# Optimization experiments

Measured on AMD Instinct MI355X. Metric: run time of the kernel, lower is better.

Reference implementation:

```python
import jax, jax.numpy as jnp
import numpy as np

B, C, H, W = 64, 3, 512, 512


def setup_inputs() -> dict:
    key = jax.random.key(0)
    k1, k2, k3 = jax.random.split(key, 3)
    img = jax.random.normal(k1, (B, C, H, W), dtype=jnp.float32)
    rot = jax.random.normal(k2, (B,), dtype=jnp.float32)          # radians
    trans = jax.random.normal(k3, (B, 2), dtype=jnp.float32) * 0.1
    scale = jnp.ones((B,), dtype=jnp.float32)
    return {"img": img, "rot": rot, "trans": trans, "scale": scale}


def reference(img, rot, trans, scale):
    # Batched equivalent of the per-image loop:
    #   theta = [[cos/s, -sin/s, tx], [sin/s, cos/s, ty]]  (2x3 per image)
    #   grid  = F.affine_grid(theta, img.size())           (align_corners=False)
    #   out   = F.grid_sample(img, grid)                    (bilinear, zeros pad)
    b_, c_, h_, w_ = img.shape
    cs = jnp.cos(rot) / scale
    sn = jnp.sin(rot) / scale

    # Base normalized grid (align_corners=False): x_i = (2i+1)/W - 1
    xs = (2.0 * jnp.arange(w_, dtype=img.dtype) + 1.0) / w_ - 1.0
    ys = (2.0 * jnp.arange(h_, dtype=img.dtype) + 1.0) / h_ - 1.0
    gy, gx = jnp.meshgrid(ys, xs, indexing="ij")  # [H, W]

    # Apply affine: [gx', gy'] = theta @ [gx, gy, 1]
    gx_t = cs[:, None, None] * gx + (-sn)[:, None, None] * gy + trans[:, 0, None, None]
    gy_t = sn[:, None, None] * gx + cs[:, None, None] * gy + trans[:, 1, None, None]

    # Unnormalize (align_corners=False): ix = ((g+1)*W - 1)/2
    ix = ((gx_t + 1.0) * w_ - 1.0) * 0.5
    iy = ((gy_t + 1.0) * h_ - 1.0) * 0.5

    x0 = jnp.floor(ix)
    y0 = jnp.floor(iy)
    wx1 = ix - x0  # frac weights
    wy1 = iy - y0
    x0i = x0.astype(jnp.int32)
    y0i = y0.astype(jnp.int32)

    bidx = jnp.arange(b_)[:, None, None]  # [B,1,1]

    def corner(yi, xi, w):
        valid = (xi >= 0) & (xi < w_) & (yi >= 0) & (yi < h_)
        yc = jnp.clip(yi, 0, h_ - 1)
        xc = jnp.clip(xi, 0, w_ - 1)
        v = img[bidx, :, yc, xc]  # [B,H,W,C] gather
        return v * (w * valid)[..., None]

    out = (
        corner(y0i, x0i, (1.0 - wy1) * (1.0 - wx1))
        + corner(y0i, x0i + 1, (1.0 - wy1) * wx1)
        + corner(y0i + 1, x0i, wy1 * (1.0 - wx1))
        + corner(y0i + 1, x0i + 1, wy1 * wx1)
    )
    return jnp.transpose(out, (0, 3, 1, 2))  # [B,C,H,W]
```

## Files before the change

kernel.cpp:

```cpp
#include <hip/hip_runtime.h>
#include <stdint.h>

#define BB 64
#define CC 3
#define HH 512
#define WW 512
#define TILE 32
#define MAXBH 48
#define MAXBW 52
#define LSTR 53

typedef float f32x2 __attribute__((ext_vector_type(2)));

__device__ __forceinline__ void pix2in(float x, float y,
                                       float cs, float sn, float tx, float ty,
                                       float& ix, float& iy)
{
    float gx = (2.0f * x + 1.0f) * (1.0f / (float)WW) - 1.0f;
    float gy = (2.0f * y + 1.0f) * (1.0f / (float)HH) - 1.0f;
    float gxt = cs * gx - sn * gy + tx;
    float gyt = sn * gx + cs * gy + ty;
    ix = ((gxt + 1.0f) * (float)WW - 1.0f) * 0.5f;
    iy = ((gyt + 1.0f) * (float)HH - 1.0f) * 0.5f;
}

__global__ __launch_bounds__(256) void warp_setup(
    const float* __restrict__ rot, const float* __restrict__ trans,
    const float* __restrict__ scale, float* __restrict__ ws)
{
    const int i = blockIdx.x * 256 + threadIdx.x;
    const int b = i >> 8, t = i & 255;
    const float r = rot[b];
    const float inv_s = 1.0f / scale[b];
    const float cs = cosf(r) * inv_s;
    const float sn = sinf(r) * inv_s;
    const float tx = trans[2 * b], ty = trans[2 * b + 1];
    if (t == 0)
        reinterpret_cast<float4*>(ws)[b] = make_float4(cs, sn, tx, ty);

    const int oy0 = (t >> 4) * TILE;
    const int ox0 = (t & 15) * TILE;
    float ixa, iya, ixb, iyb, ixc, iyc, ixd, iyd;
    pix2in((float)ox0,              (float)oy0,              cs, sn, tx, ty, ixa, iya);
    pix2in((float)(ox0 + TILE - 1), (float)oy0,              cs, sn, tx, ty, ixb, iyb);
    pix2in((float)ox0,              (float)(oy0 + TILE - 1), cs, sn, tx, ty, ixc, iyc);
    pix2in((float)(ox0 + TILE - 1), (float)(oy0 + TILE - 1), cs, sn, tx, ty, ixd, iyd);
    const float minix = fminf(fminf(ixa, ixb), fminf(ixc, ixd));
    const float maxix = fmaxf(fmaxf(ixa, ixb), fmaxf(ixc, ixd));
    const float miniy = fminf(fminf(iya, iyb), fminf(iyc, iyd));
    const float maxiy = fmaxf(fmaxf(iya, iyb), fmaxf(iyc, iyd));
    const int bx0 = (int)floorf(minix) - 1;
    const int bx1 = (int)floorf(maxix) + 2;
    const int by0 = (int)floorf(miniy) - 1;
    const int by1 = (int)floorf(maxiy) + 2;
    int bx0c = bx0 & ~3;
    const int bw = bx1 - bx0c + 1;
    const int bh = by1 - by0 + 1;

    const uint32_t fit      = (bw <= MAXBW && bh <= MAXBH) ? 1u : 0u;
    const uint32_t interior = (bx0c >= 0 && bx1 < WW && by0 >= 0 && by1 < HH) ? 1u : 0u;
    const int bx0s = min(max(bx0c, -2048), 2047);
    const int by0s = min(max(by0,  -2048), 2047);
    const int bhs  = min(bh, 63);
    const uint32_t desc = ((uint32_t)bx0s & 0xFFFu)
                        | (((uint32_t)by0s & 0xFFFu) << 12)
                        | ((uint32_t)bhs << 24)
                        | (fit << 30) | (interior << 31);
    reinterpret_cast<uint32_t*>(ws)[256 + i] = desc;
}

template <bool INTERIOR>
__device__ __forceinline__ void compute_store(
    const float (*lds)[MAXBH][LSTR], float* __restrict__ outb,
    int tid, int ox0, int oy0, int bx0c, int by0,
    float cs, float sn, float tpx, float tpy, long plane)
{
    const int row = tid >> 4;
    const int xp  = (tid & 15) * 2;
    const int oy  = oy0 + row;
    const int oxb = ox0 + xp;

    float ix0, iy0;
    pix2in((float)oxb, (float)oy, cs, sn, tpx, tpy, ix0, iy0);

    f32x2 res[CC];
    #pragma unroll
    for (int e = 0; e < 2; ++e) {
        const float ix = fmaf((float)e, cs, ix0);
        const float iy = fmaf((float)e, sn, iy0);
        const float x0f = floorf(ix), y0f = floorf(iy);
        const float wx1 = ix - x0f,  wy1 = iy - y0f;
        const float wx0 = 1.0f - wx1, wy0 = 1.0f - wy1;
        const int x0 = (int)x0f, y0 = (int)y0f;

        float w00 = wy0 * wx0, w01 = wy0 * wx1, w10 = wy1 * wx0, w11 = wy1 * wx1;
        if (!INTERIOR) {
            const int x1 = x0 + 1, y1 = y0 + 1;
            const float vx0 = (x0 >= 0 && x0 < WW) ? 1.0f : 0.0f;
            const float vx1 = (x1 >= 0 && x1 < WW) ? 1.0f : 0.0f;
            const float vy0 = (y0 >= 0 && y0 < HH) ? 1.0f : 0.0f;
            const float vy1 = (y1 >= 0 && y1 < HH) ? 1.0f : 0.0f;
            w00 *= vy0 * vx0; w01 *= vy0 * vx1; w10 *= vy1 * vx0; w11 *= vy1 * vx1;
        }

        const int idx = (y0 - by0) * LSTR + (x0 - bx0c);
        #pragma unroll
        for (int c = 0; c < CC; ++c) {
            const float* pb = &lds[c][0][0] + idx;
            res[c][e] = w00 * pb[0] + w01 * pb[1]
                      + w10 * pb[LSTR] + w11 * pb[LSTR + 1];
        }
    }
    const long ob = (long)oy * WW + oxb;
    #pragma unroll
    for (int c = 0; c < CC; ++c)
        __builtin_nontemporal_store(res[c],
            reinterpret_cast<f32x2*>(outb + (long)c * plane + ob));
}

__global__ __launch_bounds__(512) void warp_tiled(
    const float* __restrict__ img, const float* __restrict__ ws,
    float* __restrict__ out)
{
    __shared__ float lds[CC][MAXBH][LSTR];

    const int g   = blockIdx.x;
    const int swz = (g & 7) * ((BB * 256) / 8) + (g >> 3);
    const int b   = swz >> 8;
    const int t   = swz & 255;
    const int oy0 = (t >> 4) * TILE;
    const int ox0 = (t & 15) * TILE;

    const float4 p = reinterpret_cast<const float4*>(ws)[b];
    const float cs = p.x, sn = p.y, tpx = p.z, tpy = p.w;
    const uint32_t desc = reinterpret_cast<const uint32_t*>(ws)[256 + swz];
    const int  bx0c     = ((int)(desc << 20)) >> 20;
    const int  by0      = ((int)(desc << 8))  >> 20;
    const int  bh       = (desc >> 24) & 63;
    const bool fit      = (desc >> 30) & 1;
    const bool interior = (desc >> 31) & 1;

    const long plane = (long)HH * WW;
    const float* imb = img + (long)b * CC * plane;
    float* outb      = out + (long)b * CC * plane;
    const int tid = threadIdx.x;

    if (fit) {
        const int q  = tid >> 4;
        const int ql = tid & 15;
        if (ql < 13) {
            if (interior) {
                const float* prow = imb + (long)(by0 + q) * WW + bx0c + ql * 4;
                #pragma unroll
                for (int c = 0; c < CC; ++c) {
                    const float* pr = prow + (long)c * plane;
                    if (q < bh) {
                        const float4 v = *reinterpret_cast<const float4*>(pr);
                        float* dst = &lds[c][q][ql * 4];
                        dst[0] = v.x; dst[1] = v.y; dst[2] = v.z; dst[3] = v.w;
                    }
                    if (q + 32 < bh) {
                        const float4 v = *reinterpret_cast<const float4*>(pr + 32 * WW);
                        float* dst = &lds[c][q + 32][ql * 4];
                        dst[0] = v.x; dst[1] = v.y; dst[2] = v.z; dst[3] = v.w;
                    }
                }
            } else {
                #pragma unroll
                for (int c = 0; c < CC; ++c) {
                    const float* pc = imb + (long)c * plane;
                    for (int r = q; r < bh; r += 32) {
                        const int grow = by0 + r;
                        const int gcol = bx0c + ql * 4;
                        float4 v = make_float4(0.f, 0.f, 0.f, 0.f);
                        if (grow >= 0 && grow < HH) {
                            const float* prow = pc + (long)grow * WW;
                            if (gcol >= 0 && gcol <= WW - 4) {
                                v = *reinterpret_cast<const float4*>(prow + gcol);
                            } else {
                                int gc0 = gcol, gc1 = gcol + 1, gc2 = gcol + 2, gc3 = gcol + 3;
                                v.x = (gc0 >= 0 && gc0 < WW) ? prow[gc0] : 0.f;
                                v.y = (gc1 >= 0 && gc1 < WW) ? prow[gc1] : 0.f;
                                v.z = (gc2 >= 0 && gc2 < WW) ? prow[gc2] : 0.f;
                                v.w = (gc3 >= 0 && gc3 < WW) ? prow[gc3] : 0.f;
                            }
                        }
                        float* dst = &lds[c][r][ql * 4];
                        dst[0] = v.x; dst[1] = v.y; dst[2] = v.z; dst[3] = v.w;
                    }
                }
            }
        }
        __syncthreads();

        if (interior)
            compute_store<true >(lds, outb, tid, ox0, oy0, bx0c, by0, cs, sn, tpx, tpy, plane);
        else
            compute_store<false>(lds, outb, tid, ox0, oy0, bx0c, by0, cs, sn, tpx, tpy, plane);
    } else {
        #pragma unroll
        for (int k = 0; k < 2; ++k) {
            const int pidx = tid + k * 512;
            const int py = pidx >> 5;
            const int px = pidx & 31;
            const int ox = ox0 + px, oy = oy0 + py;

            float ix, iy;
            pix2in((float)ox, (float)oy, cs, sn, tpx, tpy, ix, iy);
            const float x0f = floorf(ix), y0f = floorf(iy);
            const float wx1 = ix - x0f,  wy1 = iy - y0f;
            const int x0 = (int)x0f, y0 = (int)y0f;
            const int x1 = x0 + 1,  y1 = y0 + 1;

            const float vx0 = (x0 >= 0 && x0 < WW) ? 1.0f : 0.0f;
            const float vx1 = (x1 >= 0 && x1 < WW) ? 1.0f : 0.0f;
            const float vy0 = (y0 >= 0 && y0 < HH) ? 1.0f : 0.0f;
            const float vy1 = (y1 >= 0 && y1 < HH) ? 1.0f : 0.0f;

            const int x0c = min(max(x0, 0), WW - 1);
            const int x1c = min(max(x1, 0), WW - 1);
            const int y0c = min(max(y0, 0), HH - 1);
            const int y1c = min(max(y1, 0), HH - 1);

            const float w00 = (1.0f - wy1) * (1.0f - wx1) * vy0 * vx0;
            const float w01 = (1.0f - wy1) * wx1          * vy0 * vx1;
            const float w10 = wy1          * (1.0f - wx1) * vy1 * vx0;
            const float w11 = wy1          * wx1          * vy1 * vx1;

            const int o00 = y0c * WW + x0c, o01 = y0c * WW + x1c;
            const int o10 = y1c * WW + x0c, o11 = y1c * WW + x1c;
            const int ob = oy * WW + ox;
            #pragma unroll
            for (int c = 0; c < CC; ++c) {
                const float* pc = imb + (long)c * plane;
                const float v = w00 * pc[o00] + w01 * pc[o01]
                              + w10 * pc[o10] + w11 * pc[o11];
                __builtin_nontemporal_store(v, &outb[(long)c * plane + ob]);
            }
        }
    }
}

extern "C" void kernel_launch(void* const* d_in, const int* in_sizes, int n_in,
                              void* d_out, int out_size, void* d_ws, size_t ws_size,
                              hipStream_t stream) {
    const float* img   = (const float*)d_in[0];
    const float* rot   = (const float*)d_in[1];
    const float* trans = (const float*)d_in[2];
    const float* scale = (const float*)d_in[3];
    float* out = (float*)d_out;
    float* ws  = (float*)d_ws;

    warp_setup<<<dim3(BB), 256, 0, stream>>>(rot, trans, scale, ws);
    warp_tiled<<<dim3(BB * 256), 512, 0, stream>>>(img, ws, out);
}
```

Measured before the change: 77.68 us.

## Interleave channels in LDS as float4 texels with XOR swizzle

Changes the shared-memory tile from three planar channel arrays into one interleaved array of float4 texels (RGB plus padding), stored with an XOR swizzle to spread bank accesses. Each bilinear tap now takes a single 128-bit LDS read for all three channels instead of three scalar reads, so the number of LDS instructions in the sampling loop drops. The cost is a larger LDS footprint (a padding lane per texel), which may reduce occupancy, plus a transpose during the tile load. The edge-case load path now also does scalar global loads per element.

New measurement: 76.90 us. Within noise of the previous version (-1.0%).

```diff
diff --git a/kernel.cpp b/kernel.cpp
--- a/kernel.cpp
+++ b/kernel.cpp
@@ -8,9 +8,10 @@
 #define TILE 32
 #define MAXBH 48
 #define MAXBW 52
-#define LSTR 53
+#define RS 58
 
 typedef float f32x2 __attribute__((ext_vector_type(2)));
+typedef float f32x4 __attribute__((ext_vector_type(4)));
 
 __device__ __forceinline__ void pix2in(float x, float y,
                                        float cs, float sn, float tx, float ty,
@@ -71,7 +72,7 @@
 
 template <bool INTERIOR>
 __device__ __forceinline__ void compute_store(
-    const float (*lds)[MAXBH][LSTR], float* __restrict__ outb,
+    const f32x4 (*lds)[RS], float* __restrict__ outb,
     int tid, int ox0, int oy0, int bx0c, int by0,
     float cs, float sn, float tpx, float tpy, long plane)
 {
@@ -83,7 +84,7 @@
     float ix0, iy0;
     pix2in((float)oxb, (float)oy, cs, sn, tpx, tpy, ix0, iy0);
 
-    f32x2 res[CC];
+    f32x4 acc0, acc1;
     #pragma unroll
     for (int e = 0; e < 2; ++e) {
         const float ix = fmaf((float)e, cs, ix0);
@@ -103,26 +104,34 @@
             w00 *= vy0 * vx0; w01 *= vy0 * vx1; w10 *= vy1 * vx0; w11 *= vy1 * vx1;
         }
 
-        const int idx = (y0 - by0) * LSTR + (x0 - bx0c);
-        #pragma unroll
-        for (int c = 0; c < CC; ++c) {
-            const float* pb = &lds[c][0][0] + idx;
-            res[c][e] = w00 * pb[0] + w01 * pb[1]
-                      + w10 * pb[LSTR] + w11 * pb[LSTR + 1];
-        }
+        const int lx0 = x0 - bx0c;
+        const int lx1 = lx0 + 1;
+        const int ly0 = y0 - by0;
+        const int s0  = lx0 ^ ((lx0 >> 2) & 7);
+        const int s1  = lx1 ^ ((lx1 >> 2) & 7);
+
+        const f32x4 p00 = lds[ly0][s0];
+        const f32x4 p01 = lds[ly0][s1];
+        const f32x4 p10 = lds[ly0 + 1][s0];
+        const f32x4 p11 = lds[ly0 + 1][s1];
+
+        const f32x4 r4 = w00 * p00 + w01 * p01 + w10 * p10 + w11 * p11;
+        if (e == 0) acc0 = r4; else acc1 = r4;
     }
     const long ob = (long)oy * WW + oxb;
-    #pragma unroll
-    for (int c = 0; c < CC; ++c)
-        __builtin_nontemporal_store(res[c],
-            reinterpret_cast<f32x2*>(outb + (long)c * plane + ob));
+    const f32x2 o0 = {acc0.x, acc1.x};
+    const f32x2 o1 = {acc0.y, acc1.y};
+    const f32x2 o2 = {acc0.z, acc1.z};
+    __builtin_nontemporal_store(o0, reinterpret_cast<f32x2*>(outb + ob));
+    __builtin_nontemporal_store(o1, reinterpret_cast<f32x2*>(outb + plane + ob));
+    __builtin_nontemporal_store(o2, reinterpret_cast<f32x2*>(outb + 2 * plane + ob));
 }
 
 __global__ __launch_bounds__(512) void warp_tiled(
     const float* __restrict__ img, const float* __restrict__ ws,
     float* __restrict__ out)
 {
-    __shared__ float lds[CC][MAXBH][LSTR];
+    __shared__ f32x4 lds[MAXBH][RS];
 
     const int g   = blockIdx.x;
     const int swz = (g & 7) * ((BB * 256) / 8) + (g >> 3);
@@ -149,44 +158,35 @@
         const int q  = tid >> 4;
         const int ql = tid & 15;
         if (ql < 13) {
-            if (interior) {
-                const float* prow = imb + (long)(by0 + q) * WW + bx0c + ql * 4;
-                #pragma unroll
-                for (int c = 0; c < CC; ++c) {
-                    const float* pr = prow + (long)c * plane;
-                    if (q < bh) {
-                        const float4 v = *reinterpret_cast<const float4*>(pr);
-                        float* dst = &lds[c][q][ql * 4];
-                        dst[0] = v.x; dst[1] = v.y; dst[2] = v.z; dst[3] = v.w;
-                    }
-                    if (q + 32 < bh) {
-                        const float4 v = *reinterpret_cast<const float4*>(pr + 32 * WW);
-                        float* dst = &lds[c][q + 32][ql * 4];
-                        dst[0] = v.x; dst[1] = v.y; dst[2] = v.z; dst[3] = v.w;
-                    }
+            const int sb = (ql * 4) ^ (ql & 7);
+            if (interior && (bx0c + 51 < WW)) {
+                for (int r = q; r < bh; r += 32) {
+                    const float* pr = imb + (long)(by0 + r) * WW + (bx0c + ql * 4);
+                    const float4 a  = *reinterpret_cast<const float4*>(pr);
+                    const float4 bv = *reinterpret_cast<const float4*>(pr + plane);
+                    const float4 cv = *reinterpret_cast<const float4*>(pr + 2 * plane);
+                    f32x4* lrow = lds[r];
+                    lrow[sb ^ 0] = f32x4{a.x, bv.x, cv.x, 0.f};
+                    lrow[sb ^ 1] = f32x4{a.y, bv.y, cv.y, 0.f};
+                    lrow[sb ^ 2] = f32x4{a.z, bv.z, cv.z, 0.f};
+                    lrow[sb ^ 3] = f32x4{a.w, bv.w, cv.w, 0.f};
                 }
             } else {
-                #pragma unroll
-                for (int c = 0; c < CC; ++c) {
-                    const float* pc = imb + (long)c * plane;
-                    for (int r = q; r < bh; r += 32) {
-                        const int grow = by0 + r;
-                        const int gcol = bx0c + ql * 4;
-                        float4 v = make_float4(0.f, 0.f, 0.f, 0.f);
-                        if (grow >= 0 && grow < HH) {
-                            const float* prow = pc + (long)grow * WW;
-                            if (gcol >= 0 && gcol <= WW - 4) {
-                                v = *reinterpret_cast<const float4*>(prow + gcol);
-                            } else {
-                                int gc0 = gcol, gc1 = gcol + 1, gc2 = gcol + 2, gc3 = gcol + 3;
-                                v.x = (gc0 >= 0 && gc0 < WW) ? prow[gc0] : 0.f;
-                                v.y = (gc1 >= 0 && gc1 < WW) ? prow[gc1] : 0.f;
-                                v.z = (gc2 >= 0 && gc2 < WW) ? prow[gc2] : 0.f;
-                                v.w = (gc3 >= 0 && gc3 < WW) ? prow[gc3] : 0.f;
-                            }
+                for (int r = q; r < bh; r += 32) {
+                    const int grow = by0 + r;
+                    const bool rowok = (grow >= 0) && (grow < HH);
+                    const float* pr = imb + (long)grow * WW;
+                    f32x4* lrow = lds[r];
+                    #pragma unroll
+                    for (int k = 0; k < 4; ++k) {
+                        const int gcol = bx0c + ql * 4 + k;
+                        f32x4 pv = {0.f, 0.f, 0.f, 0.f};
+                        if (rowok && gcol >= 0 && gcol < WW) {
+                            pv.x = pr[gcol];
+                            pv.y = pr[(long)gcol + plane];
+                            pv.z = pr[(long)gcol + 2 * plane];
                         }
-                        float* dst = &lds[c][r][ql * 4];
-                        dst[0] = v.x; dst[1] = v.y; dst[2] = v.z; dst[3] = v.w;
+                        lrow[sb ^ k] = pv;
                     }
                 }
             }
```
